# Optimization experiments

Measured on AMD Instinct MI355X. Metric: run time of the kernel, lower is better.

The kernel has to match this reference:

```python
import jax, jax.numpy as jnp
import numpy as np

B, T, N, H = 4, 10, 4096, 32
SR = 1.0  # sample_rate


def setup_inputs() -> dict:
    key = jax.random.key(0)
    ks = jax.random.split(key, 10)
    inputs = jax.random.normal(ks[0], (B, T, N), jnp.float32)
    states = jax.random.normal(ks[1], (T, B, N * H), jnp.float32) * 0.1
    dtw = jax.random.uniform(ks[2], (N, N), dtype=jnp.float32)
    spec_lap = jax.random.uniform(ks[3], (N, N), dtype=jnp.float32)
    laplacian = jax.random.uniform(ks[4], (N, N), dtype=jnp.float32)
    time_delay = jax.random.uniform(ks[5], (N, N), dtype=jnp.float32) * T
    W1 = jax.random.normal(ks[6], (H + 1, 2 * H), jnp.float32) * 0.05
    b1 = jnp.ones((2 * H,), jnp.float32)  # bias_init 1.0 for gate conv
    W2 = jax.random.normal(ks[7], (H + 1, H), jnp.float32) * 0.05
    b2 = jnp.zeros((H,), jnp.float32)
    return dict(inputs=inputs, states=states, dtw=dtw, spec_lap=spec_lap,
                laplacian=laplacian, time_delay=time_delay,
                W1=W1, b1=b1, W2=W2, b2=b2)


def _graph_conv(A, x, h, W, b):
    # x: [B,N], h: [B,N*H], A: [N,N] -> [B, N*out]
    conc = jnp.concatenate([x[:, :, None], h.reshape(B, N, H)], axis=2)  # [B,N,H+1]
    ac = jnp.einsum('mn,bnk->bmk', A, conc)                              # [B,N,H+1]
    out = ac @ W + b                                                     # [B,N,out]
    return out.reshape(B, -1)


def reference(inputs, states, dtw, spec_lap, laplacian, time_delay, W1, b1, W2, b2):
    eye = jnp.eye(N, dtype=jnp.float32)
    td = jnp.ceil(jnp.abs(time_delay) / SR)
    time_indicator = jnp.float32(T) - td  # tm - td with tm = times

    def step(carry, xs):
        gcn1, gcn2, _ = carry
        t, x_t, h_t = xs
        # time-based masking of dtw entries
        dtwt = jnp.where((dtw != 0) & (t + 1.0 > time_indicator), dtw, 0.0)
        multi = t == jnp.float32(T - 1)
        A = jnp.where(multi,
                      (dtwt + eye + laplacian + spec_lap) / 3.0,
                      (dtwt + spec_lap + eye) / 2.0)
        gcn1 = gcn1 + _graph_conv(A, x_t, h_t, W1, b1)       # [B, N*2H] (accumulated)
        ru = jax.nn.sigmoid(gcn1)
        r, u = jnp.split(ru, 2, axis=1)                      # flat split, as torch.chunk
        gcn2 = gcn2 + _graph_conv(A, x_t, r * h_t, W2, b2)   # [B, N*H]
        c = jnp.tanh(gcn2)
        h_new = u * h_t + (1.0 - u) * c
        return (gcn1, gcn2, h_new), None

    gcn1_0 = jnp.zeros((B, N * 2 * H), jnp.float32)
    gcn2_0 = jnp.zeros((B, N * H), jnp.float32)
    h0 = jnp.zeros((B, N * H), jnp.float32)
    ts = jnp.arange(T, dtype=jnp.float32)
    xs = (ts, jnp.transpose(inputs, (1, 0, 2)), states)  # per-step (t, x_t[B,N], h_t[B,N*H])
    (_, _, h_new), _ = jax.lax.scan(step, (gcn1_0, gcn2_0, h0), xs)
    return h_new  # [B, N*H]
```

## Files before the change

### kernel.cpp

```cpp
#include <hip/hip_runtime.h>
#include <math.h>

#define BB 4
#define TT 10
#define NN 4096
#define HH 32
#define JP 144
#define NJ2 (NN*JP)
#define NH (NN*HH)
#define NPAIR (NN*NN/2)

typedef __attribute__((ext_vector_type(8))) short short8;
typedef __attribute__((ext_vector_type(8))) _Float16 half8;
typedef __attribute__((ext_vector_type(4))) float floatx4;
typedef __attribute__((ext_vector_type(4))) unsigned int uintx4;
typedef __attribute__((ext_vector_type(2))) unsigned int uintx2;

__device__ inline unsigned short f2h(float f) {
    _Float16 h = (_Float16)f;
    unsigned short u; __builtin_memcpy(&u, &h, 2);
    return u;
}
__device__ inline unsigned pk2(float a, float b) {
    return (unsigned)f2h(a) | ((unsigned)f2h(b) << 16);
}

__global__ void k_pack(const float* __restrict__ dtw, const float* __restrict__ tdl,
                       const float* __restrict__ spl, const float* __restrict__ lap,
                       unsigned* __restrict__ Aoff, unsigned* __restrict__ Aon,
                       unsigned* __restrict__ A9, unsigned short* __restrict__ thr2) {
    int e = blockIdx.x * 256 + threadIdx.x;
    if (e >= NPAIR) return;
    size_t gi = (size_t)e * 2;
    int row = (int)(gi >> 12);
    int c0 = (int)(gi & 4095);
    float2 d = ((const float2*)dtw)[e];
    float2 td = ((const float2*)tdl)[e];
    float2 s = ((const float2*)spl)[e];
    float2 l = ((const float2*)lap)[e];
    float td0 = ceilf(fabsf(td.x)), td1 = ceilf(fabsf(td.y));
    int th0 = 10 - (int)td0; if (th0 < 0) th0 = 0;
    int th1 = 10 - (int)td1; if (th1 < 0) th1 = 0;
    float off0 = s.x + ((row == c0) ? 1.f : 0.f);
    float off1 = s.y + ((row == c0 + 1) ? 1.f : 0.f);
    float on0 = off0 + d.x, on1 = off1 + d.y;
    float a90 = off0 + l.x + ((td0 > 0.f && d.x != 0.f) ? d.x : 0.f);
    float a91 = off1 + l.y + ((td1 > 0.f && d.y != 0.f) ? d.y : 0.f);
    Aoff[e] = pk2(off0, off1);
    Aon[e]  = pk2(on0, on1);
    A9[e]   = pk2(a90, a91);
    thr2[e] = (unsigned short)(th0 | (th1 << 8));
}

__global__ void k_zpad(unsigned short* __restrict__ Ct) {
    int e = blockIdx.x * 256 + threadIdx.x;
    if (e >= TT * 12 * NN) return;
    int n = e & 4095;
    int r = e >> 12;
    int t = r / 12, j = 132 + (r % 12);
    Ct[(size_t)(t * JP + j) * NN + n] = 0;
}

__global__ void k_build_ct1(const float* __restrict__ inp, const float* __restrict__ st,
                            unsigned short* __restrict__ Ct) {
    int nb = blockIdx.x, b = blockIdx.y, t = blockIdx.z;
    int tid = threadIdx.x;
    float sc = (t == TT - 1) ? (1.f / 3.f) : 0.5f;
    int kk = tid & 31;
    int ng = tid >> 5;
    const float* stb = st + (size_t)(t * BB + b) * NH;
    unsigned short* crow = Ct + (size_t)(t * JP + b * 33 + 1 + kk) * NN;
    int n0 = nb * 128 + ng * 16;
#pragma unroll
    for (int i = 0; i < 16; i++) {
        int n = n0 + i;
        crow[n] = f2h(stb[n * 32 + kk] * sc);
    }
    if (tid < 128) {
        int n = nb * 128 + tid;
        Ct[(size_t)(t * JP + b * 33) * NN + n] = f2h(inp[((size_t)b * TT + t) * NN + n] * sc);
    }
}

__global__ void k_build_ct2(const float* __restrict__ inp, const float* __restrict__ st,
                            const float* __restrict__ G, unsigned short* __restrict__ Ct) {
    int nb = blockIdx.x, b = blockIdx.y, t = blockIdx.z;
    int tid = threadIdx.x;
    float sc = (t == TT - 1) ? (1.f / 3.f) : 0.5f;
    int kk = tid & 31;
    int ng = tid >> 5;
    const float* stb = st + (size_t)(t * BB + b) * NH;
    const float* Gb = G + (size_t)(t * BB + b) * NN * 64;
    unsigned short* crow = Ct + (size_t)(t * JP + b * 33 + 1 + kk) * NN;
    int n0 = nb * 128 + ng * 16;
#pragma unroll
    for (int i = 0; i < 16; i++) {
        int n = n0 + i;
        int jj = n * 32 + kk;
        float g = Gb[jj];
        float r = 1.0f / (1.0f + expf(-g));
        crow[n] = f2h(r * stb[jj] * sc);
    }
    if (tid < 128) {
        int n = nb * 128 + tid;
        Ct[(size_t)(t * JP + b * 33) * NN + n] = f2h(inp[((size_t)b * TT + t) * NN + n] * sc);
    }
}

__global__ __launch_bounds__(256) void k_mfma(const unsigned* __restrict__ Aoff,
                                              const unsigned* __restrict__ Aon,
                                              const unsigned* __restrict__ A9,
                                              const unsigned short* __restrict__ thr2,
                                              const unsigned* __restrict__ Ct,
                                              float* __restrict__ Out) {
    int t = blockIdx.z;
    int ks = blockIdx.y;
    int m0 = blockIdx.x * 128;
    int k0 = ks * 2048;
    int tid = threadIdx.x;
    int w = tid >> 6, lane = tid & 63;
    int lm = lane & 15, q = lane >> 4;

    __shared__ short As[2][128 * 40];
    __shared__ short Cs[2][JP * 40];

    floatx4 acc[2][9];
#pragma unroll
    for (int i = 0; i < 2; i++)
#pragma unroll
        for (int j = 0; j < 9; j++) acc[i][j] = (floatx4){0.f, 0.f, 0.f, 0.f};

    const bool last = (t == TT - 1);

    const int arow0 = tid >> 2;
    const int arow1 = arow0 + 64;
    const int ac = (tid & 3) * 4;
    const size_t kbase = (size_t)(k0 >> 1);
    const size_t ga0 = (size_t)(m0 + arow0) * 2048 + kbase + ac;
    const size_t ga1 = (size_t)(m0 + arow1) * 2048 + kbase + ac;
    const int cj0 = arow0;
    const int cj1 = arow0 + 64;
    const int cj2 = arow0 + 128;
    const unsigned* CtT = Ct + (size_t)t * JP * 2048 + kbase;

    uintx4 pO0, pO1, pA0, pA1, rC0, rC1, rC2;
    uintx2 pT0, pT1;

    auto LOADS = [&](int ku) {
        if (last) {
            pO0 = *(const uintx4*)(A9 + ga0 + ku);
            pO1 = *(const uintx4*)(A9 + ga1 + ku);
        } else {
            pO0 = *(const uintx4*)(Aoff + ga0 + ku);
            pA0 = *(const uintx4*)(Aon  + ga0 + ku);
            pT0 = *(const uintx2*)(thr2 + ga0 + ku);
            pO1 = *(const uintx4*)(Aoff + ga1 + ku);
            pA1 = *(const uintx4*)(Aon  + ga1 + ku);
            pT1 = *(const uintx2*)(thr2 + ga1 + ku);
        }
        rC0 = *(const uintx4*)(CtT + (size_t)cj0 * 2048 + ku + ac);
        rC1 = *(const uintx4*)(CtT + (size_t)cj1 * 2048 + ku + ac);
        if (tid < 64) rC2 = *(const uintx4*)(CtT + (size_t)cj2 * 2048 + ku + ac);
    };

    auto SEL = [&](uintx4& dst, const uintx4& po, const uintx4& pa, const uintx2& pt) {
#pragma unroll
        for (int u = 0; u < 4; u++) {
            unsigned th = ((u < 2) ? pt[0] : pt[1]) >> ((u & 1) * 16);
            unsigned lo = ((int)(th & 255u) <= t) ? pa[u] : po[u];
            unsigned hi = ((int)((th >> 8) & 255u) <= t) ? pa[u] : po[u];
            dst[u] = (lo & 0xFFFFu) | (hi & 0xFFFF0000u);
        }
    };

    LOADS(0);
    int p = 0;
    for (int kb = 0; kb < 64; kb++) {
        short* Asb = As[p];
        short* Csb = Cs[p];
        unsigned* Asu = (unsigned*)Asb;
        unsigned* Csu = (unsigned*)Csb;
        uintx4 r0, r1;
        if (last) { r0 = pO0; r1 = pO1; }
        else { SEL(r0, pO0, pA0, pT0); SEL(r1, pO1, pA1, pT1); }
        *(uintx4*)(Asu + arow0 * 20 + ac) = r0;
        *(uintx4*)(Asu + arow1 * 20 + ac) = r1;
        *(uintx4*)(Csu + cj0 * 20 + ac) = rC0;
        *(uintx4*)(Csu + cj1 * 20 + ac) = rC1;
        if (tid < 64) *(uintx4*)(Csu + cj2 * 20 + ac) = rC2;
        if (kb < 63) LOADS((kb + 1) * 16);
        asm volatile("s_waitcnt lgkmcnt(0)" ::: "memory");
        __builtin_amdgcn_s_barrier();
        asm volatile("" ::: "memory");
        const short* Ab = Asb;
        const short* Cb = Csb;
        short8 a0v = *(const short8*)(Ab + (w * 32 + lm) * 40 + q * 8);
        short8 a1v = *(const short8*)(Ab + (w * 32 + 16 + lm) * 40 + q * 8);
        half8 ah0 = __builtin_bit_cast(half8, a0v);
        half8 ah1 = __builtin_bit_cast(half8, a1v);
#pragma unroll
        for (int jt = 0; jt < 9; jt++) {
            short8 bv = *(const short8*)(Cb + (jt * 16 + lm) * 40 + q * 8);
            half8 bh = __builtin_bit_cast(half8, bv);
            acc[0][jt] = __builtin_amdgcn_mfma_f32_16x16x32_f16(ah0, bh, acc[0][jt], 0, 0, 0);
            acc[1][jt] = __builtin_amdgcn_mfma_f32_16x16x32_f16(ah1, bh, acc[1][jt], 0, 0, 0);
        }
        p ^= 1;
    }
    float* Ob = Out + ((size_t)ks * TT + t) * (size_t)NN * JP;
#pragma unroll
    for (int mt = 0; mt < 2; mt++) {
        int row = m0 + w * 32 + mt * 16 + q * 4;
#pragma unroll
        for (int jt = 0; jt < 9; jt++) {
            int col = jt * 16 + lm;
#pragma unroll
            for (int r = 0; r < 4; r++)
                Ob[(size_t)(row + r) * JP + col] = acc[mt][jt][r];
        }
    }
}

__global__ void k_prefix(float* __restrict__ O0, const float* __restrict__ O1) {
    int e = blockIdx.x * 256 + threadIdx.x;
    if (e >= NJ2) return;
    float run = 0.f;
#pragma unroll
    for (int t = 0; t < TT; t++) {
        run += O0[(size_t)t * NJ2 + e] + O1[(size_t)t * NJ2 + e];
        O0[(size_t)t * NJ2 + e] = run;
    }
}

__global__ __launch_bounds__(256) void k_gcn1(const float* __restrict__ P,
                                              const float* __restrict__ W1,
                                              const float* __restrict__ b1,
                                              float* __restrict__ G) {
    int m0 = blockIdx.x * 32;
    int b = blockIdx.y, t = blockIdx.z;
    int tid = threadIdx.x;
    __shared__ float Ws[33 * 64];
    __shared__ float Ps[32 * 33];
    for (int l = tid; l < 33 * 64; l += 256) Ws[l] = W1[l];
    for (int l = tid; l < 32 * 33; l += 256) {
        int mr = l / 33, kk = l - mr * 33;
        Ps[l] = P[(size_t)(t * NN + m0 + mr) * JP + b * 33 + kk];
    }
    __syncthreads();
    int qq = tid & 63, ms = tid >> 6;
    float bias = (float)(t + 1) * b1[qq];
    for (int mi = 0; mi < 8; mi++) {
        int ml = ms * 8 + mi;
        float a = bias;
#pragma unroll
        for (int kk = 0; kk < 33; kk++) a = fmaf(Ps[ml * 33 + kk], Ws[kk * 64 + qq], a);
        G[(size_t)((t * BB + b) * NN + m0 + ml) * 64 + qq] = a;
    }
}

__global__ void k_reduce(const float* __restrict__ O0, const float* __restrict__ O1,
                         float* __restrict__ S) {
    int e = blockIdx.x * 256 + threadIdx.x;
    if (e >= NJ2) return;
    float s = 0.f;
#pragma unroll
    for (int t = 0; t < TT; t++)
        s += O0[(size_t)t * NJ2 + e] + O1[(size_t)t * NJ2 + e];
    S[e] = s;
}

__global__ __launch_bounds__(256) void k_final(const float* __restrict__ S,
                                               const float* __restrict__ G,
                                               const float* __restrict__ st,
                                               const float* __restrict__ W2,
                                               const float* __restrict__ b2,
                                               float* __restrict__ out) {
    __shared__ float Ws[33 * 32];
    int tid = threadIdx.x;
    for (int l = tid; l < 33 * 32; l += 256) Ws[l] = W2[l];
    __syncthreads();
    int e = blockIdx.x * 256 + tid;
    int b = e >> 17;
    int jj = e & (NH - 1);
    int m = jj >> 5, q = jj & 31;
    float a = 10.0f * b2[q];
#pragma unroll
    for (int kk = 0; kk < 33; kk++) a = fmaf(S[m * JP + b * 33 + kk], Ws[kk * 32 + q], a);
    float c = tanhf(a);
    float gu = G[(size_t)((9 * BB + b) * NN + 2048 + (jj >> 6)) * 64 + (jj & 63)];
    float u = 1.0f / (1.0f + expf(-gu));
    float h = st[(size_t)(9 * BB + b) * NH + jj];
    out[e] = u * h + (1.0f - u) * c;
}

extern "C" void kernel_launch(void* const* d_in, const int* in_sizes, int n_in,
                              void* d_out, int out_size, void* d_ws, size_t ws_size,
                              hipStream_t stream) {
    const float* inp = (const float*)d_in[0];
    const float* st  = (const float*)d_in[1];
    const float* dtw = (const float*)d_in[2];
    const float* spl = (const float*)d_in[3];
    const float* lap = (const float*)d_in[4];
    const float* tdl = (const float*)d_in[5];
    const float* W1  = (const float*)d_in[6];
    const float* b1  = (const float*)d_in[7];
    const float* W2  = (const float*)d_in[8];
    const float* b2  = (const float*)d_in[9];
    float* out = (float*)d_out;

    char* W = (char*)d_ws;
    unsigned*       Aoff = (unsigned*)W;                     W += (size_t)NPAIR * 4;
    unsigned*       Aon  = (unsigned*)W;                     W += (size_t)NPAIR * 4;
    unsigned*       A9   = (unsigned*)W;                     W += (size_t)NPAIR * 4;
    unsigned short* thr2 = (unsigned short*)W;               W += (size_t)NPAIR * 2;
    unsigned short* Ct   = (unsigned short*)W;               W += (size_t)TT * JP * NN * 2;
    float*          O    = (float*)W;                        W += (size_t)2 * TT * NJ2 * 4;
    float*          G    = (float*)W;                        W += (size_t)TT * BB * NN * 64 * 4;
    float*          S    = (float*)W;                        W += (size_t)NJ2 * 4;
    float* O1 = O + (size_t)TT * NJ2;

    k_pack<<<NPAIR / 256, 256, 0, stream>>>(dtw, tdl, spl, lap, Aoff, Aon, A9, thr2);
    k_zpad<<<(TT * 12 * NN + 255) / 256, 256, 0, stream>>>(Ct);

    dim3 gbld(NN / 128, BB, TT);
    k_build_ct1<<<gbld, 256, 0, stream>>>(inp, st, Ct);

    dim3 gmm(NN / 128, 2, TT);
    k_mfma<<<gmm, 256, 0, stream>>>(Aoff, Aon, A9, thr2, (const unsigned*)Ct, O);

    k_prefix<<<NJ2 / 256, 256, 0, stream>>>(O, O1);

    dim3 ggcn(NN / 32, BB, TT);
    k_gcn1<<<ggcn, 256, 0, stream>>>(O, W1, b1, G);

    k_build_ct2<<<gbld, 256, 0, stream>>>(inp, st, G, Ct);

    k_mfma<<<gmm, 256, 0, stream>>>(Aoff, Aon, A9, thr2, (const unsigned*)Ct, O);

    k_reduce<<<NJ2 / 256, 256, 0, stream>>>(O, O1, S);

    k_final<<<(BB * NN * HH) / 256, 256, 0, stream>>>(S, G, st, W2, b2, out);
}
```

Baseline: 626.1 us.

## Fuse weight projection into GEMM epilogue and merge prep kernels

The GEMM epilogue now stages accumulators through shared memory and applies W1 or W2 directly, writing projected gate values (pass 1) or atomically accumulating candidate values across time and K-splits (pass 2). This replaces the separate prefix, gcn1, reduce and W2-in-final steps, using linearity so the projection happens before the time prefix sum. Packing, zero-padding and the first Ct build are merged into one prep launch. In exchange, pass 1 writes a wider 64-channel intermediate, the epilogue does per-thread scalar FMAs with global W reads, and pass 2 relies on float atomics, which makes summation order nondeterministic.

```diff
diff --git a/kernel.cpp b/kernel.cpp
--- a/kernel.cpp
+++ b/kernel.cpp
@@ -6,9 +6,9 @@
 #define NN 4096
 #define HH 32
 #define JP 144
-#define NJ2 (NN*JP)
 #define NH (NN*HH)
 #define NPAIR (NN*NN/2)
+#define QPL (BB*NN*64)
 
 typedef __attribute__((ext_vector_type(8))) short short8;
 typedef __attribute__((ext_vector_type(8))) _Float16 half8;
@@ -25,60 +25,60 @@
     return (unsigned)f2h(a) | ((unsigned)f2h(b) << 16);
 }
 
-__global__ void k_pack(const float* __restrict__ dtw, const float* __restrict__ tdl,
+__global__ void k_prep(const float* __restrict__ dtw, const float* __restrict__ tdl,
                        const float* __restrict__ spl, const float* __restrict__ lap,
+                       const float* __restrict__ inp, const float* __restrict__ st,
                        unsigned* __restrict__ Aoff, unsigned* __restrict__ Aon,
-                       unsigned* __restrict__ A9, unsigned short* __restrict__ thr2) {
-    int e = blockIdx.x * 256 + threadIdx.x;
-    if (e >= NPAIR) return;
-    size_t gi = (size_t)e * 2;
-    int row = (int)(gi >> 12);
-    int c0 = (int)(gi & 4095);
-    float2 d = ((const float2*)dtw)[e];
-    float2 td = ((const float2*)tdl)[e];
-    float2 s = ((const float2*)spl)[e];
-    float2 l = ((const float2*)lap)[e];
-    float td0 = ceilf(fabsf(td.x)), td1 = ceilf(fabsf(td.y));
-    int th0 = 10 - (int)td0; if (th0 < 0) th0 = 0;
-    int th1 = 10 - (int)td1; if (th1 < 0) th1 = 0;
-    float off0 = s.x + ((row == c0) ? 1.f : 0.f);
-    float off1 = s.y + ((row == c0 + 1) ? 1.f : 0.f);
-    float on0 = off0 + d.x, on1 = off1 + d.y;
-    float a90 = off0 + l.x + ((td0 > 0.f && d.x != 0.f) ? d.x : 0.f);
-    float a91 = off1 + l.y + ((td1 > 0.f && d.y != 0.f) ? d.y : 0.f);
-    Aoff[e] = pk2(off0, off1);
-    Aon[e]  = pk2(on0, on1);
-    A9[e]   = pk2(a90, a91);
-    thr2[e] = (unsigned short)(th0 | (th1 << 8));
-}
-
-__global__ void k_zpad(unsigned short* __restrict__ Ct) {
-    int e = blockIdx.x * 256 + threadIdx.x;
-    if (e >= TT * 12 * NN) return;
-    int n = e & 4095;
-    int r = e >> 12;
-    int t = r / 12, j = 132 + (r % 12);
-    Ct[(size_t)(t * JP + j) * NN + n] = 0;
-}
-
-__global__ void k_build_ct1(const float* __restrict__ inp, const float* __restrict__ st,
-                            unsigned short* __restrict__ Ct) {
-    int nb = blockIdx.x, b = blockIdx.y, t = blockIdx.z;
+                       unsigned* __restrict__ A9, unsigned short* __restrict__ thr2,
+                       unsigned short* __restrict__ Ct) {
+    int bx = blockIdx.x;
     int tid = threadIdx.x;
-    float sc = (t == TT - 1) ? (1.f / 3.f) : 0.5f;
-    int kk = tid & 31;
-    int ng = tid >> 5;
-    const float* stb = st + (size_t)(t * BB + b) * NH;
-    unsigned short* crow = Ct + (size_t)(t * JP + b * 33 + 1 + kk) * NN;
-    int n0 = nb * 128 + ng * 16;
-#pragma unroll
-    for (int i = 0; i < 16; i++) {
-        int n = n0 + i;
-        crow[n] = f2h(stb[n * 32 + kk] * sc);
-    }
-    if (tid < 128) {
-        int n = nb * 128 + tid;
-        Ct[(size_t)(t * JP + b * 33) * NN + n] = f2h(inp[((size_t)b * TT + t) * NN + n] * sc);
+    if (bx < NPAIR / 256) {
+        int e = bx * 256 + tid;
+        size_t gi = (size_t)e * 2;
+        int row = (int)(gi >> 12);
+        int c0 = (int)(gi & 4095);
+        float2 d = ((const float2*)dtw)[e];
+        float2 td = ((const float2*)tdl)[e];
+        float2 s = ((const float2*)spl)[e];
+        float2 l = ((const float2*)lap)[e];
+        float td0 = ceilf(fabsf(td.x)), td1 = ceilf(fabsf(td.y));
+        int th0 = 10 - (int)td0; if (th0 < 0) th0 = 0;
+        int th1 = 10 - (int)td1; if (th1 < 0) th1 = 0;
+        float off0 = s.x + ((row == c0) ? 1.f : 0.f);
+        float off1 = s.y + ((row == c0 + 1) ? 1.f : 0.f);
+        float on0 = off0 + d.x, on1 = off1 + d.y;
+        float a90 = off0 + l.x + ((td0 > 0.f && d.x != 0.f) ? d.x : 0.f);
+        float a91 = off1 + l.y + ((td1 > 0.f && d.y != 0.f) ? d.y : 0.f);
+        Aoff[e] = pk2(off0, off1);
+        Aon[e]  = pk2(on0, on1);
+        A9[e]   = pk2(a90, a91);
+        thr2[e] = (unsigned short)(th0 | (th1 << 8));
+    } else {
+        int r = bx - NPAIR / 256;
+        int nb = r & 31, b = (r >> 5) & 3, t = r >> 7;
+        float sc = (t == TT - 1) ? (1.f / 3.f) : 0.5f;
+        int kk = tid & 31;
+        int ng = tid >> 5;
+        const float* stb = st + (size_t)(t * BB + b) * NH;
+        unsigned short* crow = Ct + (size_t)(t * JP + b * 33 + 1 + kk) * NN;
+        int n0 = nb * 128 + ng * 16;
+#pragma unroll
+        for (int i = 0; i < 16; i++) {
+            int n = n0 + i;
+            crow[n] = f2h(stb[n * 32 + kk] * sc);
+        }
+        if (tid < 128) {
+            int n = nb * 128 + tid;
+            Ct[(size_t)(t * JP + b * 33) * NN + n] = f2h(inp[((size_t)b * TT + t) * NN + n] * sc);
+        }
+        if (b == 0) {
+            for (int l = tid; l < 12 * 128; l += 256) {
+                int j = 132 + (l >> 7);
+                int n = nb * 128 + (l & 127);
+                Ct[(size_t)(t * JP + j) * NN + n] = 0;
+            }
+        }
     }
 }
 
@@ -107,35 +107,25 @@
     }
 }
 
-__global__ __launch_bounds__(256) void k_mfma(const unsigned* __restrict__ Aoff,
-                                              const unsigned* __restrict__ Aon,
-                                              const unsigned* __restrict__ A9,
-                                              const unsigned short* __restrict__ thr2,
-                                              const unsigned* __restrict__ Ct,
-                                              float* __restrict__ Out) {
-    int t = blockIdx.z;
-    int ks = blockIdx.y;
-    int m0 = blockIdx.x * 128;
-    int k0 = ks * 2048;
-    int tid = threadIdx.x;
+__device__ __forceinline__ void gemm_core(
+        int t, int ks, int m0, int tid,
+        const unsigned* __restrict__ Aoff, const unsigned* __restrict__ Aon,
+        const unsigned* __restrict__ A9, const unsigned short* __restrict__ thr2,
+        const unsigned* __restrict__ Ct, short* __restrict__ As, short* __restrict__ Cs,
+        floatx4 (&acc)[2][9]) {
     int w = tid >> 6, lane = tid & 63;
     int lm = lane & 15, q = lane >> 4;
 
-    __shared__ short As[2][128 * 40];
-    __shared__ short Cs[2][JP * 40];
-
-    floatx4 acc[2][9];
 #pragma unroll
     for (int i = 0; i < 2; i++)
 #pragma unroll
         for (int j = 0; j < 9; j++) acc[i][j] = (floatx4){0.f, 0.f, 0.f, 0.f};
 
     const bool last = (t == TT - 1);
-
     const int arow0 = tid >> 2;
     const int arow1 = arow0 + 64;
     const int ac = (tid & 3) * 4;
-    const size_t kbase = (size_t)(k0 >> 1);
+    const size_t kbase = (size_t)ks * 1024;
     const size_t ga0 = (size_t)(m0 + arow0) * 2048 + kbase + ac;
     const size_t ga1 = (size_t)(m0 + arow1) * 2048 + kbase + ac;
     const int cj0 = arow0;
@@ -176,8 +166,8 @@
     LOADS(0);
     int p = 0;
     for (int kb = 0; kb < 64; kb++) {
-        short* Asb = As[p];
-        short* Csb = Cs[p];
+        short* Asb = As + p * 5120;
+        short* Csb = Cs + p * 5760;
         unsigned* Asu = (unsigned*)Asb;
         unsigned* Csu = (unsigned*)Csb;
         uintx4 r0, r1;
@@ -192,100 +182,119 @@
         asm volatile("s_waitcnt lgkmcnt(0)" ::: "memory");
         __builtin_amdgcn_s_barrier();
         asm volatile("" ::: "memory");
-        const short* Ab = Asb;
-        const short* Cb = Csb;
-        short8 a0v = *(const short8*)(Ab + (w * 32 + lm) * 40 + q * 8);
-        short8 a1v = *(const short8*)(Ab + (w * 32 + 16 + lm) * 40 + q * 8);
+        short8 a0v = *(const short8*)(Asb + (w * 32 + lm) * 40 + q * 8);
+        short8 a1v = *(const short8*)(Asb + (w * 32 + 16 + lm) * 40 + q * 8);
         half8 ah0 = __builtin_bit_cast(half8, a0v);
         half8 ah1 = __builtin_bit_cast(half8, a1v);
 #pragma unroll
         for (int jt = 0; jt < 9; jt++) {
-            short8 bv = *(const short8*)(Cb + (jt * 16 + lm) * 40 + q * 8);
+            short8 bv = *(const short8*)(Csb + (jt * 16 + lm) * 40 + q * 8);
             half8 bh = __builtin_bit_cast(half8, bv);
             acc[0][jt] = __builtin_amdgcn_mfma_f32_16x16x32_f16(ah0, bh, acc[0][jt], 0, 0, 0);
             acc[1][jt] = __builtin_amdgcn_mfma_f32_16x16x32_f16(ah1, bh, acc[1][jt], 0, 0, 0);
         }
         p ^= 1;
     }
-    float* Ob = Out + ((size_t)ks * TT + t) * (size_t)NN * JP;
+}
+
+template <int PASS>
+__global__ __launch_bounds__(256) void k_mfma(const unsigned* __restrict__ Aoff,
+                                              const unsigned* __restrict__ Aon,
+                                              const unsigned* __restrict__ A9,
+                                              const unsigned short* __restrict__ thr2,
+                                              const unsigned* __restrict__ Ct,
+                                              const float* __restrict__ Wm,
+                                              float* __restrict__ dst) {
+    int t = blockIdx.z;
+    int ks = blockIdx.y;
+    int m0 = blockIdx.x * 128;
+    int tid = threadIdx.x;
+    int w = tid >> 6, lane = tid & 63;
+    int lm = lane & 15, q = lane >> 4;
+
+    __shared__ __align__(16) short smem[21760];
+    short* As = smem;
+    short* Cs = smem + 10240;
+
+    floatx4 acc[2][9];
+    gemm_core(t, ks, m0, tid, Aoff, Aon, A9, thr2, Ct, As, Cs, acc);
+
+    __syncthreads();
+    float* Pw = (float*)smem + w * (16 * 148);
+    const int rr = lane >> 2, bq = lane & 3;
+
 #pragma unroll
     for (int mt = 0; mt < 2; mt++) {
-        int row = m0 + w * 32 + mt * 16 + q * 4;
-#pragma unroll
-        for (int jt = 0; jt < 9; jt++) {
-            int col = jt * 16 + lm;
+        __syncthreads();
+#pragma unroll
+        for (int jt = 0; jt < 9; jt++)
 #pragma unroll
             for (int r = 0; r < 4; r++)
-                Ob[(size_t)(row + r) * JP + col] = acc[mt][jt][r];
-        }
-    }
-}
-
-__global__ void k_prefix(float* __restrict__ O0, const float* __restrict__ O1) {
+                Pw[(q * 4 + r) * 148 + jt * 16 + lm] = acc[mt][jt][r];
+        float P[33];
+#pragma unroll
+        for (int kk = 0; kk < 33; kk++) P[kk] = Pw[rr * 148 + bq * 33 + kk];
+        int grow = m0 + w * 32 + mt * 16 + rr;
+        if (PASS == 1) {
+            float* drow = dst + ((size_t)(ks * TT + t) * 4 + bq) * (size_t)(NN * 64)
+                              + (size_t)grow * 64;
+#pragma unroll
+            for (int qc = 0; qc < 4; qc++) {
+                float o[16];
+#pragma unroll
+                for (int qi = 0; qi < 16; qi++) o[qi] = 0.f;
+                for (int kk = 0; kk < 33; kk++) {
+                    float pv = P[kk];
+                    const float* wrow = Wm + kk * 64 + qc * 16;
+#pragma unroll
+                    for (int qi = 0; qi < 16; qi++) o[qi] = fmaf(pv, wrow[qi], o[qi]);
+                }
+#pragma unroll
+                for (int qi = 0; qi < 16; qi++) drow[qc * 16 + qi] = o[qi];
+            }
+        } else {
+            float* frow = dst + (size_t)bq * (size_t)(NN * 32) + (size_t)grow * 32;
+#pragma unroll
+            for (int qc = 0; qc < 2; qc++) {
+                float o[16];
+#pragma unroll
+                for (int qi = 0; qi < 16; qi++) o[qi] = 0.f;
+                for (int kk = 0; kk < 33; kk++) {
+                    float pv = P[kk];
+                    const float* wrow = Wm + kk * 32 + qc * 16;
+#pragma unroll
+                    for (int qi = 0; qi < 16; qi++) o[qi] = fmaf(pv, wrow[qi], o[qi]);
+                }
+#pragma unroll
+                for (int qi = 0; qi < 16; qi++) atomicAdd(&frow[qc * 16 + qi], o[qi]);
+            }
+        }
+    }
+}
+
+__global__ void k_mid(const float* __restrict__ Qp, const float* __restrict__ b1,
+                      float* __restrict__ G, float* __restrict__ F) {
     int e = blockIdx.x * 256 + threadIdx.x;
-    if (e >= NJ2) return;
+    float bb = b1[e & 63];
     float run = 0.f;
 #pragma unroll
     for (int t = 0; t < TT; t++) {
-        run += O0[(size_t)t * NJ2 + e] + O1[(size_t)t * NJ2 + e];
-        O0[(size_t)t * NJ2 + e] = run;
-    }
-}
-
-__global__ __launch_bounds__(256) void k_gcn1(const float* __restrict__ P,
-                                              const float* __restrict__ W1,
-                                              const float* __restrict__ b1,
-                                              float* __restrict__ G) {
-    int m0 = blockIdx.x * 32;
-    int b = blockIdx.y, t = blockIdx.z;
-    int tid = threadIdx.x;
-    __shared__ float Ws[33 * 64];
-    __shared__ float Ps[32 * 33];
-    for (int l = tid; l < 33 * 64; l += 256) Ws[l] = W1[l];
-    for (int l = tid; l < 32 * 33; l += 256) {
-        int mr = l / 33, kk = l - mr * 33;
-        Ps[l] = P[(size_t)(t * NN + m0 + mr) * JP + b * 33 + kk];
-    }
-    __syncthreads();
-    int qq = tid & 63, ms = tid >> 6;
-    float bias = (float)(t + 1) * b1[qq];
-    for (int mi = 0; mi < 8; mi++) {
-        int ml = ms * 8 + mi;
-        float a = bias;
-#pragma unroll
-        for (int kk = 0; kk < 33; kk++) a = fmaf(Ps[ml * 33 + kk], Ws[kk * 64 + qq], a);
-        G[(size_t)((t * BB + b) * NN + m0 + ml) * 64 + qq] = a;
-    }
-}
-
-__global__ void k_reduce(const float* __restrict__ O0, const float* __restrict__ O1,
-                         float* __restrict__ S) {
-    int e = blockIdx.x * 256 + threadIdx.x;
-    if (e >= NJ2) return;
-    float s = 0.f;
-#pragma unroll
-    for (int t = 0; t < TT; t++)
-        s += O0[(size_t)t * NJ2 + e] + O1[(size_t)t * NJ2 + e];
-    S[e] = s;
-}
-
-__global__ __launch_bounds__(256) void k_final(const float* __restrict__ S,
+        run += Qp[(size_t)t * QPL + e] + Qp[(size_t)(TT + t) * QPL + e];
+        G[(size_t)t * QPL + e] = (float)(t + 1) * bb + run;
+    }
+    if (e < BB * NN * 32) F[e] = 0.f;
+}
+
+__global__ __launch_bounds__(256) void k_final(const float* __restrict__ F,
                                                const float* __restrict__ G,
                                                const float* __restrict__ st,
-                                               const float* __restrict__ W2,
                                                const float* __restrict__ b2,
                                                float* __restrict__ out) {
-    __shared__ float Ws[33 * 32];
-    int tid = threadIdx.x;
-    for (int l = tid; l < 33 * 32; l += 256) Ws[l] = W2[l];
-    __syncthreads();
-    int e = blockIdx.x * 256 + tid;
+    int e = blockIdx.x * 256 + threadIdx.x;
     int b = e >> 17;
     int jj = e & (NH - 1);
-    int m = jj >> 5, q = jj & 31;
-    float a = 10.0f * b2[q];
-#pragma unroll
-    for (int kk = 0; kk < 33; kk++) a = fmaf(S[m * JP + b * 33 + kk], Ws[kk * 32 + q], a);
+    int qq = jj & 31;
+    float a = 10.0f * b2[qq] + F[e];
     float c = tanhf(a);
     float gu = G[(size_t)((9 * BB + b) * NN + 2048 + (jj >> 6)) * 64 + (jj & 63)];
     float u = 1.0f / (1.0f + expf(-gu));
@@ -314,30 +323,22 @@
     unsigned*       A9   = (unsigned*)W;                     W += (size_t)NPAIR * 4;
     unsigned short* thr2 = (unsigned short*)W;               W += (size_t)NPAIR * 2;
     unsigned short* Ct   = (unsigned short*)W;               W += (size_t)TT * JP * NN * 2;
-    float*          O    = (float*)W;                        W += (size_t)2 * TT * NJ2 * 4;
-    float*          G    = (float*)W;                        W += (size_t)TT * BB * NN * 64 * 4;
-    float*          S    = (float*)W;                        W += (size_t)NJ2 * 4;
-    float* O1 = O + (size_t)TT * NJ2;
-
-    k_pack<<<NPAIR / 256, 256, 0, stream>>>(dtw, tdl, spl, lap, Aoff, Aon, A9, thr2);
-    k_zpad<<<(TT * 12 * NN + 255) / 256, 256, 0, stream>>>(Ct);
+    float*          Qp   = (float*)W;                        W += (size_t)2 * TT * QPL * 4;
+    float*          G    = (float*)W;                        W += (size_t)TT * QPL * 4;
+    float*          F    = (float*)W;                        W += (size_t)BB * NN * 32 * 4;
+
+    k_prep<<<NPAIR / 256 + 1280, 256, 0, stream>>>(dtw, tdl, spl, lap, inp, st,
+                                                   Aoff, Aon, A9, thr2, Ct);
+
+    dim3 gmm(NN / 128, 2, TT);
+    k_mfma<1><<<gmm, 256, 0, stream>>>(Aoff, Aon, A9, thr2, (const unsigned*)Ct, W1, Qp);
+
+    k_mid<<<QPL / 256, 256, 0, stream>>>(Qp, b1, G, F);
 
     dim3 gbld(NN / 128, BB, TT);
-    k_build_ct1<<<gbld, 256, 0, stream>>>(inp, st, Ct);
-
-    dim3 gmm(NN / 128, 2, TT);
-    k_mfma<<<gmm, 256, 0, stream>>>(Aoff, Aon, A9, thr2, (const unsigned*)Ct, O);
-
-    k_prefix<<<NJ2 / 256, 256, 0, stream>>>(O, O1);
-
-    dim3 ggcn(NN / 32, BB, TT);
-    k_gcn1<<<ggcn, 256, 0, stream>>>(O, W1, b1, G);
-
     k_build_ct2<<<gbld, 256, 0, stream>>>(inp, st, G, Ct);
 
-    k_mfma<<<gmm, 256, 0, stream>>>(Aoff, Aon, A9, thr2, (const unsigned*)Ct, O);
-
-    k_reduce<<<NJ2 / 256, 256, 0, stream>>>(O, O1, S);
-
-    k_final<<<(BB * NN * HH) / 256, 256, 0, stream>>>(S, G, st, W2, b2, out);
-}
+    k_mfma<2><<<gmm, 256, 0, stream>>>(Aoff, Aon, A9, thr2, (const unsigned*)Ct, W2, F);
+
+    k_final<<<(BB * NN * HH) / 256, 256, 0, stream>>>(F, G, st, b2, out);
+}
```

New measurement: 1.148 ms. 1.83x slower.
